# Performance work log

Hardware: AMD Instinct MI355X
Metric: run time of the kernel (lower is better)

Reference implementation:

```python
import jax, jax.numpy as jnp
import numpy as np
from jax import lax

B, C, H, W = 4, 512, 48, 48
R = 8            # inter_rate -> spatial q/k channels = C // R
C4 = C // 4      # chl_attention query channels
N = H * W


def _conv1x1(x, w, b=None):
    # x: (B,C,H,W), w: (O,C)
    y = jnp.einsum('bchw,oc->bohw', x, w)
    if b is not None:
        y = y + b[None, :, None, None]
    return y


def _conv3x3(x, w):
    # w: (O,I,3,3), SAME padding, no bias
    return lax.conv_general_dilated(x, w, (1, 1), 'SAME',
                                    dimension_numbers=('NCHW', 'OIHW', 'NCHW'))


def _bn_relu(x, scale, bias):
    # eval-mode BatchNorm folded into per-channel scale/bias, then ReLU
    return jax.nn.relu(x * scale[None, :, None, None] + bias[None, :, None, None])


def _masked_softmax(e, mask):
    # softmax restricted to mask>0 positions (== exp(e)*mask / sum(exp(e)*mask))
    neg = jnp.finfo(e.dtype).min
    z = jnp.where(mask[None] > 0, e, neg)
    return jax.nn.softmax(z, axis=-1)


def _chl(x, qw, qs, qb, ew, eb):
    # channel attention block (chl_attention)
    b, c, h, w = x.shape
    n = h * w
    q = jnp.einsum('bchw,oc->bohw', x, qw)                 # (B,C4,H,W)
    q = jax.nn.relu(q * qs[None, :, None, None] + qb[None, :, None, None])
    q = q.reshape(b, C4, n)
    k = x.reshape(b, c, n)
    energy = jnp.einsum('bqn,bcn->bqc', q, k)              # (B,C4,C)
    expand = jnp.einsum('oq,bqc->boc', ew, energy) + eb[None, :, None]  # (B,C,C)
    en = jnp.max(expand, -1, keepdims=True) - expand
    attn = jax.nn.softmax(en, -1)                          # (B,C,C)
    out = jnp.einsum('bcd,bdn->bcn', attn, k)
    return out.reshape(b, c, h, w)


def setup_inputs() -> dict:
    key = jax.random.key(0)
    ks = jax.random.split(key, 32)
    f = jnp.float32
    s = lambda k, shp, sc: (sc * jax.random.normal(k, shp)).astype(f)
    inp = {}
    inp['x'] = s(ks[0], (B, C, H, W), 1.0)
    Cr = C // R
    inp['wq'] = s(ks[1], (Cr, C), 1.0 / np.sqrt(C))
    inp['bq'] = s(ks[2], (Cr,), 0.02)
    inp['wk'] = s(ks[3], (Cr, C), 1.0 / np.sqrt(C))
    inp['bk'] = s(ks[4], (Cr,), 0.02)
    inp['wv0'] = s(ks[5], (C, C), 1.0 / np.sqrt(C))
    inp['bv0'] = s(ks[6], (C,), 0.02)
    inp['conv1_w'] = s(ks[7], (C, C, 3, 3), 1.0 / np.sqrt(9 * C))
    inp['conv1_s'] = (1.0 + 0.1 * jax.random.normal(ks[8], (C,))).astype(f)
    inp['conv1_b'] = s(ks[9], (C,), 0.05)
    inp['conv2_w'] = s(ks[10], (C, C, 3, 3), 1.0 / np.sqrt(9 * C))
    inp['conv2_s'] = (1.0 + 0.1 * jax.random.normal(ks[11], (C,))).astype(f)
    inp['conv2_b'] = s(ks[12], (C,), 0.05)
    inp['gamma'] = jnp.full((1,), 0.5, f)
    inp['gamma1'] = jnp.full((1,), 0.5, f)
    inp['gamma2'] = jnp.full((1,), 0.5, f)
    # chl_attention #1 params
    inp['c1_qw'] = s(ks[13], (C4, C), 1.0 / np.sqrt(C))
    inp['c1_qs'] = (1.0 + 0.1 * jax.random.normal(ks[14], (C4,))).astype(f)
    inp['c1_qb'] = s(ks[15], (C4,), 0.05)
    inp['c1_ew'] = s(ks[16], (C, C4), 1.0 / np.sqrt(C4))
    inp['c1_eb'] = s(ks[17], (C,), 0.02)
    # chl_attention #2 params
    inp['c2_qw'] = s(ks[18], (C4, C), 1.0 / np.sqrt(C))
    inp['c2_qs'] = (1.0 + 0.1 * jax.random.normal(ks[19], (C4,))).astype(f)
    inp['c2_qb'] = s(ks[20], (C4,), 0.05)
    inp['c2_ew'] = s(ks[21], (C, C4), 1.0 / np.sqrt(C4))
    inp['c2_eb'] = s(ks[22], (C,), 0.02)
    # binary (N,N) masks: random sparsity + diagonal so every row has support
    eye = jnp.eye(N, dtype=f)
    m1 = (jax.random.uniform(ks[23], (N, N)) < 0.25).astype(f)
    m2 = (jax.random.uniform(ks[24], (N, N)) < 0.10).astype(f)
    inp['mask1'] = jnp.maximum(m1, eye)
    inp['mask2'] = jnp.maximum(m2, eye)
    return inp


def reference(x, wq, bq, wk, bk, wv0, bv0, conv1_w, conv1_s, conv1_b,
              conv2_w, conv2_s, conv2_b, gamma, gamma1, gamma2,
              c1_qw, c1_qs, c1_qb, c1_ew, c1_eb,
              c2_qw, c2_qs, c2_qb, c2_ew, c2_eb, mask1, mask2):
    b, c, h, w = x.shape
    n = h * w
    q = _conv1x1(x, wq, bq).reshape(b, -1, n)   # (B,Cr,N)
    k = _conv1x1(x, wk, bk).reshape(b, -1, n)   # (B,Cr,N)
    energy = jnp.einsum('bqn,bqm->bnm', q, k)   # (B,N,N)
    attn0 = jax.nn.softmax(energy, -1)
    attn1 = _masked_softmax(energy, mask1)
    attn2 = _masked_softmax(energy, mask2)
    v = _conv1x1(x, wv0, bv0).reshape(b, c, n)
    # pass 0 (unmasked)
    out0 = jnp.einsum('bcn,bmn->bcm', v, attn0).reshape(b, c, h, w)
    out0 = gamma[0] * out0 + x
    out0 = _bn_relu(_conv3x3(out0, conv1_w), conv1_s, conv1_b)
    # pass 1 (mask1, channel-attn value)
    v1 = _chl(out0, c1_qw, c1_qs, c1_qb, c1_ew, c1_eb).reshape(b, c, n)
    out1 = jnp.einsum('bcn,bmn->bcm', v1, attn1).reshape(b, c, h, w)
    out1 = gamma1[0] * out1 + out0
    out1 = _bn_relu(_conv3x3(out1, conv2_w), conv2_s, conv2_b)
    # pass 2 (mask2)
    v2 = _chl(out1, c2_qw, c2_qs, c2_qb, c2_ew, c2_eb).reshape(b, c, n)
    out2 = jnp.einsum('bcn,bmn->bcm', v2, attn2).reshape(b, c, h, w)
    out = gamma2[0] * out2 + out1
    return out
```

## Files before the change

### kernel.cpp

```cpp
#include <hip/hip_runtime.h>

#define B_  4
#define C_  512
#define H_  48
#define W_  48
#define N_  2304
#define CR_ 64
#define C4_ 128
#define TK  16
#define LDSP 68
#define PW  50
#define PN  2500
#define KW  4608

typedef short  s16x8 __attribute__((ext_vector_type(8)));
typedef float  f32x4 __attribute__((ext_vector_type(4)));

__device__ __forceinline__ unsigned short f2bf(float f) {
  union { float f; unsigned int u; } v; v.f = f;
  const unsigned int u = v.u;
  return (unsigned short)((u + 0x7FFFu + ((u >> 16) & 1u)) >> 16);
}
__device__ __forceinline__ float bf2f(unsigned short h) {
  union { unsigned int u; float f; } v; v.u = ((unsigned int)h) << 16;
  return v.f;
}

__device__ __forceinline__ float blockReduceMax(float v, float* red) {
  const int tid = threadIdx.x;
  red[tid] = v; __syncthreads();
  for (int s = 128; s > 0; s >>= 1) {
    if (tid < s) red[tid] = fmaxf(red[tid], red[tid + s]);
    __syncthreads();
  }
  float r = red[0]; __syncthreads();
  return r;
// ... 447 lines not shown
  unsigned short* Tlb = Tl + (size_t)b * N_ * C_;
  for (int cs = 0; cs < 8; ++cs) {
    const int c0 = cs * 64;
    __syncthreads();
#pragma unroll
    for (int i = 0; i < 16; ++i) {
      const int cc = i * 4 + (tid >> 6);
      t[cc][tid & 63] = Xb[(size_t)(c0 + cc) * N_ + n0 + (tid & 63)];
    }
    __syncthreads();
    const int cc = tid & 63;
#pragma unroll
    for (int i = 0; i < 16; ++i) {
      const int nn = i * 4 + (tid >> 6);
      const float v = t[cc][nn];
      const unsigned short hh = f2bf(v);
      Thb[(size_t)(n0 + nn) * C_ + c0 + cc] = hh;
      Tlb[(size_t)(n0 + nn) * C_ + c0 + cc] = f2bf(v - bf2f(hh));
    }
  }
}

__global__ __launch_bounds__(256)
void mfma_conv3(const unsigned short* __restrict__ Xh, const unsigned short* __restrict__ Xl,
                const unsigned short* __restrict__ Wh, const unsigned short* __restrict__ Wl,
                const float* __restrict__ sc, const float* __restrict__ bi,
                float* __restrict__ Y)
{
  __shared__ unsigned short Ah[128][72], Al[128][72];
  __shared__ unsigned short Bh[64][72], Bl[64][72];
  const int b  = blockIdx.z;
  const int m0 = blockIdx.y * 128, n0 = blockIdx.x * 64;
  const int tid  = threadIdx.x;
  const int lane = tid & 63, wave = tid >> 6;
  const int wm = wave >> 1, wn = wave & 1;
  const int lrow = lane & 15, lk8 = (lane >> 4) * 8;
  const int aRow = tid >> 1, aK = (tid & 1) * 32;
  const int bRow = tid >> 2, bK = (tid & 3) * 16;
  const int nj = n0 + bRow;
  const int pbase = (nj / 48 + 1) * PW + (nj % 48) + 1;
  const unsigned short* Xhb = Xh + (size_t)b * PN * C_;
  const unsigned short* Xlb = Xl + (size_t)b * PN * C_;
  f32x4 acc[4][2] = {};
  s16x8 a0h, a1h, a2h, a3h, a0l, a1l, a2l, a3l, b0h, b1h, b0l, b1l;

#define CONV_LD(IT)                                                             \
  {                                                                             \
    const int tap_ = (IT) >> 3, c0_ = ((IT) & 7) * 64;                          \
    const int t3_ = tap_ / 3;                                                   \
    const int toff_ = (t3_ - 1) * PW + (tap_ - t3_ * 3 - 1);                    \
    const size_t bofs_ = (size_t)(pbase + toff_) * C_ + c0_ + bK;               \
    const size_t wrow_ = (size_t)(m0 + aRow) * KW + (size_t)tap_ * C_ + c0_ + aK; \
    a0h = *(const s16x8*)(Wh + wrow_);      a1h = *(const s16x8*)(Wh + wrow_ + 8);  \
    a2h = *(const s16x8*)(Wh + wrow_ + 16); a3h = *(const s16x8*)(Wh + wrow_ + 24); \
    a0l = *(const s16x8*)(Wl + wrow_);      a1l = *(const s16x8*)(Wl + wrow_ + 8);  \
    a2l = *(const s16x8*)(Wl + wrow_ + 16); a3l = *(const s16x8*)(Wl + wrow_ + 24); \
    b0h = *(const s16x8*)(Xhb + bofs_);     b1h = *(const s16x8*)(Xhb + bofs_ + 8); \
    b0l = *(const s16x8*)(Xlb + bofs_);     b1l = *(const s16x8*)(Xlb + bofs_ + 8); \
  }

  CONV_LD(0);
  for (int it = 0; it < 72; ++it) {
    *(s16x8*)&Ah[aRow][aK]      = a0h; *(s16x8*)&Ah[aRow][aK + 8]  = a1h;
    *(s16x8*)&Ah[aRow][aK + 16] = a2h; *(s16x8*)&Ah[aRow][aK + 24] = a3h;
    *(s16x8*)&Al[aRow][aK]      = a0l; *(s16x8*)&Al[aRow][aK + 8]  = a1l;
    *(s16x8*)&Al[aRow][aK + 16] = a2l; *(s16x8*)&Al[aRow][aK + 24] = a3l;
    *(s16x8*)&Bh[bRow][bK]      = b0h; *(s16x8*)&Bh[bRow][bK + 8]  = b1h;
    *(s16x8*)&Bl[bRow][bK]      = b0l; *(s16x8*)&Bl[bRow][bK + 8]  = b1l;
    __syncthreads();
    if (it < 71) CONV_LD(it + 1);
#pragma unroll
    for (int kc = 0; kc < 2; ++kc) {
      s16x8 ah[4], al[4], bh[2], bl[2];
#pragma unroll
      for (int mt = 0; mt < 4; ++mt) {
        ah[mt] = *(const s16x8*)&Ah[wm * 64 + mt * 16 + lrow][kc * 32 + lk8];
        al[mt] = *(const s16x8*)&Al[wm * 64 + mt * 16 + lrow][kc * 32 + lk8];
      }
#pragma unroll
      for (int nt = 0; nt < 2; ++nt) {
        bh[nt] = *(const s16x8*)&Bh[wn * 32 + nt * 16 + lrow][kc * 32 + lk8];
        bl[nt] = *(const s16x8*)&Bl[wn * 32 + nt * 16 + lrow][kc * 32 + lk8];
      }
#pragma unroll
      for (int mt = 0; mt < 4; ++mt)
#pragma unroll
        for (int nt = 0; nt < 2; ++nt) {
          acc[mt][nt] = __builtin_amdgcn_mfma_f32_16x16x32_bf16(ah[mt], bh[nt], acc[mt][nt], 0, 0, 0);
          acc[mt][nt] = __builtin_amdgcn_mfma_f32_16x16x32_bf16(ah[mt], bl[nt], acc[mt][nt], 0, 0, 0);
          acc[mt][nt] = __builtin_amdgcn_mfma_f32_16x16x32_bf16(al[mt], bh[nt], acc[mt][nt], 0, 0, 0);
        }
    }
    __syncthreads();
  }
#undef CONV_LD

  float* Yb = Y + (size_t)b * C_ * N_;
#pragma unroll
  for (int mt = 0; mt < 4; ++mt)
#pragma unroll
    for (int nt = 0; nt < 2; ++nt) {
      const int col = n0 + wn * 32 + nt * 16 + lrow;
      const int rbase = m0 + wm * 64 + mt * 16 + (lane >> 4) * 4;
#pragma unroll
      for (int i = 0; i < 4; ++i) {
        const int row = rbase + i;
        const float v = fmaxf(acc[mt][nt][i] * sc[row] + bi[row], 0.f);
        Yb[(size_t)row * N_ + col] = v;
      }
    }
}

__global__ __launch_bounds__(256)
void mfma_apply(const unsigned short* __restrict__ V, const float* __restrict__ E,
                const float* __restrict__ st, int variant,
                const float* __restrict__ mask,
                const float* __restrict__ gammaPtr,
                const float* __restrict__ Resid, float* __restrict__ Y)
{
  __shared__ unsigned short As[128][72];
  __shared__ unsigned short Bs[64][72];
  const int b  = blockIdx.z;
  const int c0 = blockIdx.y * 128, m0 = blockIdx.x * 64;
  const int tid  = threadIdx.x;
  const int lane = tid & 63, wave = tid >> 6;
  const int wm = wave >> 1, wn = wave & 1;
  const int lrow = lane & 15, lk8 = (lane >> 4) * 8;
  const int aRow = tid >> 1, aK = (tid & 1) * 32;
  const int bRow = tid >> 2, bK = (tid & 3) * 16;
  const int mrow = m0 + bRow;
  const float* sp = st + ((size_t)b * N_ + mrow) * 6 + variant * 2;
  const float mx = sp[0], rs = 1.f / sp[1];
  const unsigned short* Vb = V + (size_t)b * C_ * N_;
  const float* Er = E + ((size_t)b * N_ + mrow) * N_;
  const float* Mr = mask ? mask + (size_t)mrow * N_ : nullptr;
  f32x4 acc[4][2] = {};
  s16x8 a0, a1, a2, a3;
  float4 e0, e1, e2, e3, q0, q1, q2, q3;

#define APPLY_LD(K0)                                                      \
  {                                                                       \
    const unsigned short* s = Vb + (size_t)(c0 + aRow) * N_ + (K0) + aK;  \
    a0 = *(const s16x8*)(s);      a1 = *(const s16x8*)(s + 8);            \
    a2 = *(const s16x8*)(s + 16); a3 = *(const s16x8*)(s + 24);           \
    const float* e = Er + (K0) + bK;                                      \
    e0 = *(const float4*)(e);     e1 = *(const float4*)(e + 4);           \
    e2 = *(const float4*)(e + 8); e3 = *(const float4*)(e + 12);          \
    if (Mr) {                                                             \
      const float* m = Mr + (K0) + bK;                                    \
      q0 = *(const float4*)(m);     q1 = *(const float4*)(m + 4);         \
      q2 = *(const float4*)(m + 8); q3 = *(const float4*)(m + 12);        \
    }                                                                     \
  }

  APPLY_LD(0);
  for (int k0 = 0; k0 < N_; k0 += 64) {
    *(s16x8*)&As[aRow][aK]      = a0; *(s16x8*)&As[aRow][aK + 8]  = a1;
    *(s16x8*)&As[aRow][aK + 16] = a2; *(s16x8*)&As[aRow][aK + 24] = a3;
    {
      float w[16];
      const float4 ee[4] = {e0, e1, e2, e3};
      const float4 qq[4] = {q0, q1, q2, q3};
#pragma unroll
      for (int g4 = 0; g4 < 4; ++g4) {
        const float4 e4 = ee[g4];
        w[g4 * 4 + 0] = __expf(e4.x - mx) * rs;
        w[g4 * 4 + 1] = __expf(e4.y - mx) * rs;
        w[g4 * 4 + 2] = __expf(e4.z - mx) * rs;
        w[g4 * 4 + 3] = __expf(e4.w - mx) * rs;
        if (Mr) {
          const float4 m4 = qq[g4];
          if (!(m4.x > 0.f)) w[g4 * 4 + 0] = 0.f;
          if (!(m4.y > 0.f)) w[g4 * 4 + 1] = 0.f;
          if (!(m4.z > 0.f)) w[g4 * 4 + 2] = 0.f;
          if (!(m4.w > 0.f)) w[g4 * 4 + 3] = 0.f;
        }
      }
      s16x8 p0, p1;
#pragma unroll
      for (int t = 0; t < 8; ++t) { p0[t] = (short)f2bf(w[t]); p1[t] = (short)f2bf(w[8 + t]); }
      *(s16x8*)&Bs[bRow][bK]     = p0;
      *(s16x8*)&Bs[bRow][bK + 8] = p1;
    }
    __syncthreads();
    if (k0 + 64 < N_) APPLY_LD(k0 + 64);
#pragma unroll
    for (int kc = 0; kc < 2; ++kc) {
      s16x8 av[4], bv[2];
#pragma unroll
      for (int mt = 0; mt < 4; ++mt)
        av[mt] = *(const s16x8*)&As[wm * 64 + mt * 16 + lrow][kc * 32 + lk8];
#pragma unroll
      for (int nt = 0; nt < 2; ++nt)
        bv[nt] = *(const s16x8*)&Bs[wn * 32 + nt * 16 + lrow][kc * 32 + lk8];
#pragma unroll
      for (int mt = 0; mt < 4; ++mt)
#pragma unroll
        for (int nt = 0; nt < 2; ++nt)
          acc[mt][nt] = __builtin_amdgcn_mfma_f32_16x16x32_bf16(av[mt], bv[nt], acc[mt][nt], 0, 0, 0);
    }
    __syncthreads();
  }
#undef APPLY_LD

  const float g = gammaPtr[0];
  float* Yb = Y + (size_t)b * C_ * N_;
  const float* Rb = Resid + (size_t)b * C_ * N_;
#pragma unroll
  for (int mt = 0; mt < 4; ++mt)
#pragma unroll
    for (int nt = 0; nt < 2; ++nt) {
      const int col = m0 + wn * 32 + nt * 16 + lrow;
      const int rbase = c0 + wm * 64 + mt * 16 + (lane >> 4) * 4;
#pragma unroll
      for (int i = 0; i < 4; ++i) {
        const int row = rbase + i;
        const size_t off = (size_t)row * N_ + col;
        Yb[off] = g * acc[mt][nt][i] + Rb[off];
      }
    }
}

__global__ __launch_bounds__(256)
void mfma_conv_split(const float* __restrict__ X, const float* __restrict__ Wt,
                     const float* __restrict__ sc, const float* __restrict__ bi,
                     float* __restrict__ Y)
{
  __shared__ unsigned short Ah[64][72], Al[64][72];
  __shared__ unsigned short Bh[64][72], Bl[64][72];
  const int b  = blockIdx.z;
  const int m0 = blockIdx.y * 64, n0 = blockIdx.x * 64;
  const int tid  = threadIdx.x;
  const int lane = tid & 63, wave = tid >> 6;
  const int wm = wave >> 1, wn = wave & 1;
  const int lrow = lane & 15, lk8 = (lane >> 4) * 8;
  const int sRow = tid >> 2, sK = (tid & 3) * 16;
  const int tj = tid & 63, tkg = (tid >> 6) * 16;
  const int n = n0 + tj, yy = n / W_, xx = n - yy * W_;
  const float* Xb = X + (size_t)b * C_ * N_;
  f32x4 acc[2][2] = {};

  for (int k0 = 0; k0 < KW; k0 += 64) {
    {
      const float* src = Wt + (size_t)(m0 + sRow) * KW + k0 + sK;
      unsigned short h[16], l[16];
#pragma unroll
      for (int t = 0; t < 16; ++t) {
        const float v = src[t];
        const unsigned short hh = f2bf(v);
        h[t] = hh;
        l[t] = f2bf(v - bf2f(hh));
      }
      *(s16x8*)&Ah[sRow][sK]     = *(s16x8*)&h[0];
      *(s16x8*)&Ah[sRow][sK + 8] = *(s16x8*)&h[8];
      *(s16x8*)&Al[sRow][sK]     = *(s16x8*)&l[0];
      *(s16x8*)&Al[sRow][sK + 8] = *(s16x8*)&l[8];
    }
    {
#pragma unroll
      for (int ii = 0; ii < 16; ii += 2) {
        unsigned int ph = 0, pl = 0;
#pragma unroll
        for (int hft = 0; hft < 2; ++hft) {
          const int kg = k0 + tkg + ii + hft;
          const int c = kg / 9, tap = kg - c * 9;
          const int t3 = tap / 3;
          const int iy = yy + t3 - 1, ix = xx + (tap - t3 * 3) - 1;
          float v = 0.f;
          if (iy >= 0 && iy < H_ && ix >= 0 && ix < W_)
            v = Xb[(size_t)c * N_ + iy * W_ + ix];
          const unsigned short hh = f2bf(v);
          const unsigned short ll = f2bf(v - bf2f(hh));
          ph |= ((unsigned int)hh) << (16 * hft);
          pl |= ((unsigned int)ll) << (16 * hft);
        }
        *(unsigned int*)&Bh[tj][tkg + ii] = ph;
        *(unsigned int*)&Bl[tj][tkg + ii] = pl;
      }
    }
    __syncthreads();
#pragma unroll
    for (int kc = 0; kc < 2; ++kc) {
      const s16x8 ah0 = *(const s16x8*)&Ah[wm * 32 + lrow     ][kc * 32 + lk8];
      const s16x8 ah1 = *(const s16x8*)&Ah[wm * 32 + 16 + lrow][kc * 32 + lk8];
      const s16x8 al0 = *(const s16x8*)&Al[wm * 32 + lrow     ][kc * 32 + lk8];
      const s16x8 al1 = *(const s16x8*)&Al[wm * 32 + 16 + lrow][kc * 32 + lk8];
      const s16x8 bh0 = *(const s16x8*)&Bh[wn * 32 + lrow     ][kc * 32 + lk8];
      const s16x8 bh1 = *(const s16x8*)&Bh[wn * 32 + 16 + lrow][kc * 32 + lk8];
      const s16x8 bl0 = *(const s16x8*)&Bl[wn * 32 + lrow     ][kc * 32 + lk8];
      const s16x8 bl1 = *(const s16x8*)&Bl[wn * 32 + 16 + lrow][kc * 32 + lk8];
      acc[0][0] = __builtin_amdgcn_mfma_f32_16x16x32_bf16(ah0, bh0, acc[0][0], 0, 0, 0);
      acc[0][1] = __builtin_amdgcn_mfma_f32_16x16x32_bf16(ah0, bh1, acc[0][1], 0, 0, 0);
      acc[1][0] = __builtin_amdgcn_mfma_f32_16x16x32_bf16(ah1, bh0, acc[1][0], 0, 0, 0);
      acc[1][1] = __builtin_amdgcn_mfma_f32_16x16x32_bf16(ah1, bh1, acc[1][1], 0, 0, 0);
      acc[0][0] = __builtin_amdgcn_mfma_f32_16x16x32_bf16(ah0, bl0, acc[0][0], 0, 0, 0);
      acc[0][1] = __builtin_amdgcn_mfma_f32_16x16x32_bf16(ah0, bl1, acc[0][1], 0, 0, 0);
      acc[1][0] = __builtin_amdgcn_mfma_f32_16x16x32_bf16(ah1, bl0, acc[1][0], 0, 0, 0);
      acc[1][1] = __builtin_amdgcn_mfma_f32_16x16x32_bf16(ah1, bl1, acc[1][1], 0, 0, 0);
      acc[0][0] = __builtin_amdgcn_mfma_f32_16x16x32_bf16(al0, bh0, acc[0][0], 0, 0, 0);
      acc[0][1] = __builtin_amdgcn_mfma_f32_16x16x32_bf16(al0, bh1, acc[0][1], 0, 0, 0);
      acc[1][0] = __builtin_amdgcn_mfma_f32_16x16x32_bf16(al1, bh0, acc[1][0], 0, 0, 0);
      acc[1][1] = __builtin_amdgcn_mfma_f32_16x16x32_bf16(al1, bh1, acc[1][1], 0, 0, 0);
    }
    __syncthreads();
  }

  float* Yb = Y + (size_t)b * C_ * N_;
#pragma unroll
  for (int mt = 0; mt < 2; ++mt)
#pragma unroll
    for (int nt = 0; nt < 2; ++nt) {
      const int col = n0 + wn * 32 + nt * 16 + lrow;
      const int rbase = m0 + wm * 32 + mt * 16 + (lane >> 4) * 4;
#pragma unroll
      for (int i = 0; i < 4; ++i) {
        const int row = rbase + i;
        const float v = fmaxf(acc[mt][nt][i] * sc[row] + bi[row], 0.f);
        Yb[(size_t)row * N_ + col] = v;
      }
    }
}

__global__ __launch_bounds__(256)
void softmax_stats(const float* __restrict__ E, const float* __restrict__ M1,
                   const float* __restrict__ M2, float* __restrict__ st)
{
  const int row = blockIdx.x, b = blockIdx.y, tid = threadIdx.x;
  const float* er = E + ((size_t)b * N_ + row) * N_;
  const float* r1 = M1 + (size_t)row * N_;
  const float* r2 = M2 + (size_t)row * N_;
  float mx0 = -3.4e38f, mx1 = -3.4e38f, mx2 = -3.4e38f;
  for (int n = tid; n < N_; n += 256) {
    const float v = er[n];
    mx0 = fmaxf(mx0, v);
    if (r1[n] > 0.f) mx1 = fmaxf(mx1, v);
    if (r2[n] > 0.f) mx2 = fmaxf(mx2, v);
  }
  __shared__ float red[256];
  mx0 = blockReduceMax(mx0, red);
  mx1 = blockReduceMax(mx1, red);
  mx2 = blockReduceMax(mx2, red);
  float s0 = 0.f, s1 = 0.f, s2 = 0.f;
  for (int n = tid; n < N_; n += 256) {
// ... 250 lines not shown
  const float* c2ew   = (const float*)d_in[24];
  const float* c2eb   = (const float*)d_in[25];
  const float* mask1  = (const float*)d_in[26];
  const float* mask2  = (const float*)d_in[27];

  const size_t QK = 589824;
  const size_t CQ = 1179648;
  const size_t VV = 4718592;
  const size_t EE = 21233664;
  const size_t ST = 55296;
  const size_t CE = 262144;
  const size_t CA = 1048576;
  const size_t ELEMS_B = CQ + VV + EE + ST + VV + CE + CA;
  const size_t ELEMS_A = ELEMS_B + EE / 2;
  const int tier = (ws_size >= ELEMS_A * 4) ? 0
                 : (ws_size >= ELEMS_B * 4) ? 1 : 2;

  float* ws = (float*)d_ws;
  float *qbuf, *kbuf, *cq, *vbuf, *ebuf, *stb, *o0, *ce1, *cat_;
  unsigned short *Xh = nullptr, *Xl = nullptr,
                 *W1h = nullptr, *W1l = nullptr, *W2h = nullptr, *W2l = nullptr,
                 *xTh = nullptr, *xTl = nullptr, *oTh = nullptr, *oTl = nullptr;
  float *qTf = nullptr, *kTf = nullptr;
  if (tier <= 1) {
    qbuf = ws; kbuf = ws + QK;
    cq   = ws;
    vbuf = ws + CQ;
    ebuf = vbuf + VV;
    stb  = ebuf + EE;
    o0   = stb + ST;
    ce1  = o0 + VV;
    cat_ = ce1 + CE;
    if (tier == 0) {
      unsigned short* reg = (unsigned short*)(cat_ + CA);
      xTh = reg;
      xTl = reg + 4718592;
      qTf = (float*)(reg + 9437184);
      kTf = qTf + 589824;
      W1h = reg + 11796480;
      W1l = reg + 14155776;
      W2h = reg + 16515072;
      W2l = reg + 18874368;
      Xh  = reg;
      Xl  = reg + 5120000;
      oTh = reg;
      oTl = reg + 4718592;
    }
  } else {
    qbuf = ws; kbuf = qbuf + QK;
    cq   = kbuf + QK;
    vbuf = cq + CQ;
    stb  = vbuf + VV;
    o0   = stb + ST;
    ce1  = o0 + VV;
    cat_ = ce1 + CE;
    ebuf = nullptr;
  }
  float* t0 = (float*)d_out;
  unsigned short* vb16 = (unsigned short*)vbuf;

  const dim3 TPB(256);
  const long long sxc = (long long)C_ * N_;
  const long long sqr = (long long)CR_ * N_;
  const long long sq4 = (long long)C4_ * N_;
  const long long sNN = (long long)N_ * N_;
  const long long sNC = (long long)N_ * C_;
  const long long sCC = (long long)C_ * C_;
  const long long sEC = (long long)C4_ * C_;
  const long long sNR = (long long)N_ * CR_;

  if (tier == 0) {
    tr_split<<<dim3(B_, 36), TPB, 0, stream>>>(x, xTh, xTl);
    mfma_sp<<<dim3(36, 1, 4), TPB, 0, stream>>>(wq, 0, C_, xTh, xTl, sNC, C_, 1,
        qTf, sNR, CR_, 1, C_, 1, nullptr, bq, 0);
    mfma_sp<<<dim3(36, 1, 4), TPB, 0, stream>>>(wk, 0, C_, xTh, xTl, sNC, C_, 1,
        kTf, sNR, CR_, 1, C_, 1, nullptr, bk, 0);
    mfma_gemm<<<dim3(36, 8, 4), TPB, 0, stream>>>(wv0, 0, 0, C_, xTh, sNC, C_, 2,
        vb16, 1, sxc, N_, C_, nullptr, bv0, 0, nullptr, nullptr, 0);
    mfma_sp<<<dim3(36, 36, 4), TPB, 0, stream>>>(qTf, sNR, CR_, kTf, nullptr, sNR, CR_, 0,
        ebuf, sNN, N_, 0, CR_, 1, nullptr, nullptr, 0);
    softmax_stats<<<dim3(N_, 4), TPB, 0, stream>>>(ebuf, mask1, mask2, stb);
    wsplit<<<dim3(512, 9), TPB, 0, stream>>>(c1w, W1h, W1l);
    wsplit<<<dim3(512, 9), TPB, 0, stream>>>(c2w, W2h, W2l);
  } else if (tier == 1) {
    gemm_nn<<<dim3(36, 1, 4), TPB, 0, stream>>>(wq, 0, C_, x, sxc, N_,
                                                qbuf, sqr, N_, C_, nullptr, bq, 0);
    gemm_nn<<<dim3(36, 1, 4), TPB, 0, stream>>>(wk, 0, C_, x, sxc, N_,
                                                kbuf, sqr, N_, C_, nullptr, bk, 0);
    mfma_gemm<<<dim3(36, 8, 4), TPB, 0, stream>>>(wv0, 0, 0, C_, x, sxc, N_, 1,
        vbuf, 0, sxc, N_, C_, nullptr, bv0, 0, nullptr, nullptr, 0);
    gemm_tn<<<dim3(36, 36, 4), TPB, 0, stream>>>(qbuf, sqr, N_, kbuf, sqr, N_,
                                                 ebuf, sNN, N_, CR_);
    softmax_stats<<<dim3(N_, 4), TPB, 0, stream>>>(ebuf, mask1, mask2, stb);
  } else {
    gemm_nn<<<dim3(36, 1, 4), TPB, 0, stream>>>(wq, 0, C_, x, sxc, N_,
                                                qbuf, sqr, N_, C_, nullptr, bq, 0);
    gemm_nn<<<dim3(36, 1, 4), TPB, 0, stream>>>(wk, 0, C_, x, sxc, N_,
                                                kbuf, sqr, N_, C_, nullptr, bk, 0);
    mfma_gemm<<<dim3(36, 8, 4), TPB, 0, stream>>>(wv0, 0, 0, C_, x, sxc, N_, 1,
        vbuf, 0, sxc, N_, C_, nullptr, bv0, 0, nullptr, nullptr, 0);
    softmax_stats_rq<<<dim3(N_, 4), TPB, 0, stream>>>(qbuf, kbuf, mask1, mask2, stb);
  }

  for (int pass = 0; pass < 3; ++pass) {
    const float* msk = (pass == 0) ? nullptr : (pass == 1 ? mask1 : mask2);
    const float* gm  = (pass == 0) ? gamma : (pass == 1 ? gamma1 : gamma2);
    const float* res = (pass == 0) ? x : o0;
    float* dst = (pass == 2) ? (float*)d_out : t0;

    if (tier == 0) {
      mfma_apply<<<dim3(36, 4, 4), TPB, 0, stream>>>(vb16, ebuf, stb, pass, msk,
                                                     gm, res, dst);
    } else if (tier == 1) {
      attn_apply<<<dim3(36, 8, 4), TPB, 0, stream>>>(vbuf, ebuf, stb, pass, msk,
                                                     gm, res, dst);
    } else {
      attn_apply_rq<<<dim3(36, 8, 4), TPB, 0, stream>>>(vbuf, qbuf, kbuf, stb, pass, msk,
                                                        gm, res, dst);
    }
    if (pass == 2) break;

    const float* cs = (pass == 0) ? c1s : c2s;
    const float* cb = (pass == 0) ? c1b : c2b;
    if (tier == 0) {
      pad_split2<<<dim3(B_, 37), TPB, 0, stream>>>(dst, Xh, Xl);
      mfma_conv3<<<dim3(36, 4, 4), TPB, 0, stream>>>(Xh, Xl,
          (pass == 0) ? W1h : W2h, (pass == 0) ? W1l : W2l, cs, cb, o0);
    } else {
      const float* cw = (pass == 0) ? c1w : c2w;
      mfma_conv_split<<<dim3(36, 8, 4), TPB, 0, stream>>>(dst, cw, cs, cb, o0);
    }

    const float* qw = (pass == 0) ? c1qw : c2qw;
    const float* qs = (pass == 0) ? c1qs : c2qs;
    const float* qb = (pass == 0) ? c1qb : c2qb;
    const float* ew = (pass == 0) ? c1ew : c2ew;
    const float* eb = (pass == 0) ? c1eb : c2eb;
    if (tier == 0) {
      tr_split<<<dim3(B_, 36), TPB, 0, stream>>>(o0, oTh, oTl);
      mfma_sp<<<dim3(36, 2, 4), TPB, 0, stream>>>(qw, 0, C_, oTh, oTl, sNC, C_, 1,
          cq, sq4, N_, 0, C_, 1, qs, qb, 1);
      zero_buf<<<dim3(256), TPB, 0, stream>>>((float4*)ce1, (int)(CE / 4));
      mfma_sp<<<dim3(8, 2, 16), TPB, 0, stream>>>(cq, sq4, N_, o0, nullptr, sxc, N_, 0,
          ce1, sEC, C4_, 2, N_, 4, nullptr, nullptr, 0);
      mfma_sp<<<dim3(8, 8, 4), TPB, 0, stream>>>(ew, 0, C4_, ce1, nullptr, sEC, C4_, 0,
          cat_, sCC, C_, 0, C4_, 1, nullptr, eb, 0);
      chl_softmax<<<dim3(C_ * 4), TPB, 0, stream>>>(cat_);
      mfma_gemm<<<dim3(36, 8, 4), TPB, 0, stream>>>(cat_, 0, sCC, C_, oTh, sNC, C_, 2,
          vb16, 1, sxc, N_, C_, nullptr, nullptr, 0, nullptr, nullptr, 0);
// ... 15 lines not shown
```

Measured before the change: 1.283 ms.

## Pack attention masks into bitmasks and switch conv to 64-row tiles

Adds a mask_pack kernel that turns each float mask row into 64-bit ballot words. The softmax stats kernel and the attention apply kernel now read these bits instead of float masks, which cuts mask memory traffic by about 32x in the masked passes. The 3x3 conv goes back to a 64x64 output tile (mfma_conv2, grid 36x8x4) in place of the 128x64 tile, giving more blocks and fewer registers per block but less reuse of each loaded tile. Two extra small pack launches are added.

Result: faster. 1.222 ms (-4.8%).

```diff
diff --git a/kernel.cpp b/kernel.cpp
--- a/kernel.cpp
+++ b/kernel.cpp
@@ -12,6 +12,7 @@
 #define PW  50
 #define PN  2500
 #define KW  4608
+#define NW  36
 
 typedef short  s16x8 __attribute__((ext_vector_type(8)));
 typedef float  f32x4 __attribute__((ext_vector_type(4)));
@@ -505,209 +506,23 @@
 }
 
 __global__ __launch_bounds__(256)
-void mfma_conv3(const unsigned short* __restrict__ Xh, const unsigned short* __restrict__ Xl,
+void mask_pack(const float* __restrict__ M, unsigned long long* __restrict__ Mb)
+{
+  const int row = blockIdx.x;
+  const int tid = threadIdx.x, lane = tid & 63, wv = tid >> 6;
+  const float* r = M + (size_t)row * N_;
+  unsigned long long* o = Mb + (size_t)row * NW;
+  for (int i = wv; i < NW; i += 4) {
+    const unsigned long long m = __ballot(r[i * 64 + lane] > 0.f);
+    if (lane == 0) o[i] = m;
+  }
+}
+
+__global__ __launch_bounds__(256)
+void mfma_conv2(const unsigned short* __restrict__ Xh, const unsigned short* __restrict__ Xl,
                 const unsigned short* __restrict__ Wh, const unsigned short* __restrict__ Wl,
                 const float* __restrict__ sc, const float* __restrict__ bi,
                 float* __restrict__ Y)
-{
-  __shared__ unsigned short Ah[128][72], Al[128][72];
-  __shared__ unsigned short Bh[64][72], Bl[64][72];
-  const int b  = blockIdx.z;
-  const int m0 = blockIdx.y * 128, n0 = blockIdx.x * 64;
-  const int tid  = threadIdx.x;
-  const int lane = tid & 63, wave = tid >> 6;
-  const int wm = wave >> 1, wn = wave & 1;
-  const int lrow = lane & 15, lk8 = (lane >> 4) * 8;
-  const int aRow = tid >> 1, aK = (tid & 1) * 32;
-  const int bRow = tid >> 2, bK = (tid & 3) * 16;
-  const int nj = n0 + bRow;
-  const int pbase = (nj / 48 + 1) * PW + (nj % 48) + 1;
-  const unsigned short* Xhb = Xh + (size_t)b * PN * C_;
-  const unsigned short* Xlb = Xl + (size_t)b * PN * C_;
-  f32x4 acc[4][2] = {};
-  s16x8 a0h, a1h, a2h, a3h, a0l, a1l, a2l, a3l, b0h, b1h, b0l, b1l;
-
-#define CONV_LD(IT)                                                             \
-  {                                                                             \
-    const int tap_ = (IT) >> 3, c0_ = ((IT) & 7) * 64;                          \
-    const int t3_ = tap_ / 3;                                                   \
-    const int toff_ = (t3_ - 1) * PW + (tap_ - t3_ * 3 - 1);                    \
-    const size_t bofs_ = (size_t)(pbase + toff_) * C_ + c0_ + bK;               \
-    const size_t wrow_ = (size_t)(m0 + aRow) * KW + (size_t)tap_ * C_ + c0_ + aK; \
-    a0h = *(const s16x8*)(Wh + wrow_);      a1h = *(const s16x8*)(Wh + wrow_ + 8);  \
-    a2h = *(const s16x8*)(Wh + wrow_ + 16); a3h = *(const s16x8*)(Wh + wrow_ + 24); \
-    a0l = *(const s16x8*)(Wl + wrow_);      a1l = *(const s16x8*)(Wl + wrow_ + 8);  \
-    a2l = *(const s16x8*)(Wl + wrow_ + 16); a3l = *(const s16x8*)(Wl + wrow_ + 24); \
-    b0h = *(const s16x8*)(Xhb + bofs_);     b1h = *(const s16x8*)(Xhb + bofs_ + 8); \
-    b0l = *(const s16x8*)(Xlb + bofs_);     b1l = *(const s16x8*)(Xlb + bofs_ + 8); \
-  }
-
-  CONV_LD(0);
-  for (int it = 0; it < 72; ++it) {
-    *(s16x8*)&Ah[aRow][aK]      = a0h; *(s16x8*)&Ah[aRow][aK + 8]  = a1h;
-    *(s16x8*)&Ah[aRow][aK + 16] = a2h; *(s16x8*)&Ah[aRow][aK + 24] = a3h;
-    *(s16x8*)&Al[aRow][aK]      = a0l; *(s16x8*)&Al[aRow][aK + 8]  = a1l;
-    *(s16x8*)&Al[aRow][aK + 16] = a2l; *(s16x8*)&Al[aRow][aK + 24] = a3l;
-    *(s16x8*)&Bh[bRow][bK]      = b0h; *(s16x8*)&Bh[bRow][bK + 8]  = b1h;
-    *(s16x8*)&Bl[bRow][bK]      = b0l; *(s16x8*)&Bl[bRow][bK + 8]  = b1l;
-    __syncthreads();
-    if (it < 71) CONV_LD(it + 1);
-#pragma unroll
-    for (int kc = 0; kc < 2; ++kc) {
-      s16x8 ah[4], al[4], bh[2], bl[2];
-#pragma unroll
-      for (int mt = 0; mt < 4; ++mt) {
-        ah[mt] = *(const s16x8*)&Ah[wm * 64 + mt * 16 + lrow][kc * 32 + lk8];
-        al[mt] = *(const s16x8*)&Al[wm * 64 + mt * 16 + lrow][kc * 32 + lk8];
-      }
-#pragma unroll
-      for (int nt = 0; nt < 2; ++nt) {
-        bh[nt] = *(const s16x8*)&Bh[wn * 32 + nt * 16 + lrow][kc * 32 + lk8];
-        bl[nt] = *(const s16x8*)&Bl[wn * 32 + nt * 16 + lrow][kc * 32 + lk8];
-      }
-#pragma unroll
-      for (int mt = 0; mt < 4; ++mt)
-#pragma unroll
-        for (int nt = 0; nt < 2; ++nt) {
-          acc[mt][nt] = __builtin_amdgcn_mfma_f32_16x16x32_bf16(ah[mt], bh[nt], acc[mt][nt], 0, 0, 0);
-          acc[mt][nt] = __builtin_amdgcn_mfma_f32_16x16x32_bf16(ah[mt], bl[nt], acc[mt][nt], 0, 0, 0);
-          acc[mt][nt] = __builtin_amdgcn_mfma_f32_16x16x32_bf16(al[mt], bh[nt], acc[mt][nt], 0, 0, 0);
-        }
-    }
-    __syncthreads();
-  }
-#undef CONV_LD
-
-  float* Yb = Y + (size_t)b * C_ * N_;
-#pragma unroll
-  for (int mt = 0; mt < 4; ++mt)
-#pragma unroll
-    for (int nt = 0; nt < 2; ++nt) {
-      const int col = n0 + wn * 32 + nt * 16 + lrow;
-      const int rbase = m0 + wm * 64 + mt * 16 + (lane >> 4) * 4;
-#pragma unroll
-      for (int i = 0; i < 4; ++i) {
-        const int row = rbase + i;
-        const float v = fmaxf(acc[mt][nt][i] * sc[row] + bi[row], 0.f);
-        Yb[(size_t)row * N_ + col] = v;
-      }
-    }
-}
-
-__global__ __launch_bounds__(256)
-void mfma_apply(const unsigned short* __restrict__ V, const float* __restrict__ E,
-                const float* __restrict__ st, int variant,
-                const float* __restrict__ mask,
-                const float* __restrict__ gammaPtr,
-                const float* __restrict__ Resid, float* __restrict__ Y)
-{
-  __shared__ unsigned short As[128][72];
-  __shared__ unsigned short Bs[64][72];
-  const int b  = blockIdx.z;
-  const int c0 = blockIdx.y * 128, m0 = blockIdx.x * 64;
-  const int tid  = threadIdx.x;
-  const int lane = tid & 63, wave = tid >> 6;
-  const int wm = wave >> 1, wn = wave & 1;
-  const int lrow = lane & 15, lk8 = (lane >> 4) * 8;
-  const int aRow = tid >> 1, aK = (tid & 1) * 32;
-  const int bRow = tid >> 2, bK = (tid & 3) * 16;
-  const int mrow = m0 + bRow;
-  const float* sp = st + ((size_t)b * N_ + mrow) * 6 + variant * 2;
-  const float mx = sp[0], rs = 1.f / sp[1];
-  const unsigned short* Vb = V + (size_t)b * C_ * N_;
-  const float* Er = E + ((size_t)b * N_ + mrow) * N_;
-  const float* Mr = mask ? mask + (size_t)mrow * N_ : nullptr;
-  f32x4 acc[4][2] = {};
-  s16x8 a0, a1, a2, a3;
-  float4 e0, e1, e2, e3, q0, q1, q2, q3;
-
-#define APPLY_LD(K0)                                                      \
-  {                                                                       \
-    const unsigned short* s = Vb + (size_t)(c0 + aRow) * N_ + (K0) + aK;  \
-    a0 = *(const s16x8*)(s);      a1 = *(const s16x8*)(s + 8);            \
-    a2 = *(const s16x8*)(s + 16); a3 = *(const s16x8*)(s + 24);           \
-    const float* e = Er + (K0) + bK;                                      \
-    e0 = *(const float4*)(e);     e1 = *(const float4*)(e + 4);           \
-    e2 = *(const float4*)(e + 8); e3 = *(const float4*)(e + 12);          \
-    if (Mr) {                                                             \
-      const float* m = Mr + (K0) + bK;                                    \
-      q0 = *(const float4*)(m);     q1 = *(const float4*)(m + 4);         \
-      q2 = *(const float4*)(m + 8); q3 = *(const float4*)(m + 12);        \
-    }                                                                     \
-  }
-
-  APPLY_LD(0);
-  for (int k0 = 0; k0 < N_; k0 += 64) {
-    *(s16x8*)&As[aRow][aK]      = a0; *(s16x8*)&As[aRow][aK + 8]  = a1;
-    *(s16x8*)&As[aRow][aK + 16] = a2; *(s16x8*)&As[aRow][aK + 24] = a3;
-    {
-      float w[16];
-      const float4 ee[4] = {e0, e1, e2, e3};
-      const float4 qq[4] = {q0, q1, q2, q3};
-#pragma unroll
-      for (int g4 = 0; g4 < 4; ++g4) {
-        const float4 e4 = ee[g4];
-        w[g4 * 4 + 0] = __expf(e4.x - mx) * rs;
-        w[g4 * 4 + 1] = __expf(e4.y - mx) * rs;
-        w[g4 * 4 + 2] = __expf(e4.z - mx) * rs;
-        w[g4 * 4 + 3] = __expf(e4.w - mx) * rs;
-        if (Mr) {
-          const float4 m4 = qq[g4];
-          if (!(m4.x > 0.f)) w[g4 * 4 + 0] = 0.f;
-          if (!(m4.y > 0.f)) w[g4 * 4 + 1] = 0.f;
-          if (!(m4.z > 0.f)) w[g4 * 4 + 2] = 0.f;
-          if (!(m4.w > 0.f)) w[g4 * 4 + 3] = 0.f;
-        }
-      }
-      s16x8 p0, p1;
-#pragma unroll
-      for (int t = 0; t < 8; ++t) { p0[t] = (short)f2bf(w[t]); p1[t] = (short)f2bf(w[8 + t]); }
-      *(s16x8*)&Bs[bRow][bK]     = p0;
-      *(s16x8*)&Bs[bRow][bK + 8] = p1;
-    }
-    __syncthreads();
-    if (k0 + 64 < N_) APPLY_LD(k0 + 64);
-#pragma unroll
-    for (int kc = 0; kc < 2; ++kc) {
-      s16x8 av[4], bv[2];
-#pragma unroll
-      for (int mt = 0; mt < 4; ++mt)
-        av[mt] = *(const s16x8*)&As[wm * 64 + mt * 16 + lrow][kc * 32 + lk8];
-#pragma unroll
-      for (int nt = 0; nt < 2; ++nt)
-        bv[nt] = *(const s16x8*)&Bs[wn * 32 + nt * 16 + lrow][kc * 32 + lk8];
-#pragma unroll
-      for (int mt = 0; mt < 4; ++mt)
-#pragma unroll
-        for (int nt = 0; nt < 2; ++nt)
-          acc[mt][nt] = __builtin_amdgcn_mfma_f32_16x16x32_bf16(av[mt], bv[nt], acc[mt][nt], 0, 0, 0);
-    }
-    __syncthreads();
-  }
-#undef APPLY_LD
-
-  const float g = gammaPtr[0];
-  float* Yb = Y + (size_t)b * C_ * N_;
-  const float* Rb = Resid + (size_t)b * C_ * N_;
-#pragma unroll
-  for (int mt = 0; mt < 4; ++mt)
-#pragma unroll
-    for (int nt = 0; nt < 2; ++nt) {
-      const int col = m0 + wn * 32 + nt * 16 + lrow;
-      const int rbase = c0 + wm * 64 + mt * 16 + (lane >> 4) * 4;
-#pragma unroll
-      for (int i = 0; i < 4; ++i) {
-        const int row = rbase + i;
-        const size_t off = (size_t)row * N_ + col;
-        Yb[off] = g * acc[mt][nt][i] + Rb[off];
-      }
-    }
-}
-
-__global__ __launch_bounds__(256)
-void mfma_conv_split(const float* __restrict__ X, const float* __restrict__ Wt,
-                     const float* __restrict__ sc, const float* __restrict__ bi,
-                     float* __restrict__ Y)
 {
   __shared__ unsigned short Ah[64][72], Al[64][72];
   __shared__ unsigned short Bh[64][72], Bl[64][72];
@@ -718,50 +533,34 @@
   const int wm = wave >> 1, wn = wave & 1;
   const int lrow = lane & 15, lk8 = (lane >> 4) * 8;
   const int sRow = tid >> 2, sK = (tid & 3) * 16;
-  const int tj = tid & 63, tkg = (tid >> 6) * 16;
-  const int n = n0 + tj, yy = n / W_, xx = n - yy * W_;
-  const float* Xb = X + (size_t)b * C_ * N_;
+  const int nj = n0 + sRow;
+  const int pbase = (nj / 48 + 1) * PW + (nj % 48) + 1;
+  const unsigned short* Xhb = Xh + (size_t)b * PN * C_;
+  const unsigned short* Xlb = Xl + (size_t)b * PN * C_;
   f32x4 acc[2][2] = {};
-
-  for (int k0 = 0; k0 < KW; k0 += 64) {
-    {
-      const float* src = Wt + (size_t)(m0 + sRow) * KW + k0 + sK;
-      unsigned short h[16], l[16];
-#pragma unroll
-      for (int t = 0; t < 16; ++t) {
-        const float v = src[t];
-        const unsigned short hh = f2bf(v);
-        h[t] = hh;
-        l[t] = f2bf(v - bf2f(hh));
-      }
-      *(s16x8*)&Ah[sRow][sK]     = *(s16x8*)&h[0];
-      *(s16x8*)&Ah[sRow][sK + 8] = *(s16x8*)&h[8];
-      *(s16x8*)&Al[sRow][sK]     = *(s16x8*)&l[0];
-      *(s16x8*)&Al[sRow][sK + 8] = *(s16x8*)&l[8];
-    }
-    {
-#pragma unroll
-      for (int ii = 0; ii < 16; ii += 2) {
-        unsigned int ph = 0, pl = 0;
-#pragma unroll
-        for (int hft = 0; hft < 2; ++hft) {
-          const int kg = k0 + tkg + ii + hft;
-          const int c = kg / 9, tap = kg - c * 9;
-          const int t3 = tap / 3;
-          const int iy = yy + t3 - 1, ix = xx + (tap - t3 * 3) - 1;
-          float v = 0.f;
-          if (iy >= 0 && iy < H_ && ix >= 0 && ix < W_)
-            v = Xb[(size_t)c * N_ + iy * W_ + ix];
-          const unsigned short hh = f2bf(v);
-          const unsigned short ll = f2bf(v - bf2f(hh));
-          ph |= ((unsigned int)hh) << (16 * hft);
-          pl |= ((unsigned int)ll) << (16 * hft);
-        }
-        *(unsigned int*)&Bh[tj][tkg + ii] = ph;
-        *(unsigned int*)&Bl[tj][tkg + ii] = pl;
-      }
-    }
-    __syncthreads();
+  s16x8 r0, r1, r2, r3, r4, r5, r6, r7;
+
+#define CONV_LD(IT)                                                        \
+  {                                                                        \
+    const int tap_ = (IT) >> 3, c0_ = ((IT) & 7) * 64;                     \
+    const int t3_ = tap_ / 3;                                              \
+    const int toff_ = (t3_ - 1) * PW + (tap_ - t3_ * 3 - 1);               \
+    const size_t bofs_ = (size_t)(pbase + toff_) * C_ + c0_ + sK;          \
+    const size_t wrow_ = (size_t)(m0 + sRow) * KW + (size_t)tap_ * C_ + c0_ + sK; \
+    r0 = *(const s16x8*)(Wh + wrow_);     r1 = *(const s16x8*)(Wh + wrow_ + 8); \
+    r2 = *(const s16x8*)(Wl + wrow_);     r3 = *(const s16x8*)(Wl + wrow_ + 8); \
+    r4 = *(const s16x8*)(Xhb + bofs_);    r5 = *(const s16x8*)(Xhb + bofs_ + 8); \
+    r6 = *(const s16x8*)(Xlb + bofs_);    r7 = *(const s16x8*)(Xlb + bofs_ + 8); \
+  }
+
+  CONV_LD(0);
+  for (int it = 0; it < 72; ++it) {
+    *(s16x8*)&Ah[sRow][sK] = r0; *(s16x8*)&Ah[sRow][sK + 8] = r1;
+    *(s16x8*)&Al[sRow][sK] = r2; *(s16x8*)&Al[sRow][sK + 8] = r3;
+    *(s16x8*)&Bh[sRow][sK] = r4; *(s16x8*)&Bh[sRow][sK + 8] = r5;
+    *(s16x8*)&Bl[sRow][sK] = r6; *(s16x8*)&Bl[sRow][sK + 8] = r7;
+    __syncthreads();
+    if (it < 71) CONV_LD(it + 1);
 #pragma unroll
     for (int kc = 0; kc < 2; ++kc) {
       const s16x8 ah0 = *(const s16x8*)&Ah[wm * 32 + lrow     ][kc * 32 + lk8];
@@ -787,6 +586,7 @@
     }
     __syncthreads();
   }
+#undef CONV_LD
 
   float* Yb = Y + (size_t)b * C_ * N_;
 #pragma unroll
@@ -802,6 +602,255 @@
         Yb[(size_t)row * N_ + col] = v;
       }
     }
+}
+
+__global__ __launch_bounds__(256)
+void mfma_apply(const unsigned short* __restrict__ V, const float* __restrict__ E,
+                const float* __restrict__ st, int variant,
+                const unsigned long long* __restrict__ Mb,
+                const float* __restrict__ gammaPtr,
+                const float* __restrict__ Resid, float* __restrict__ Y)
+{
+  __shared__ unsigned short As[128][72];
+  __shared__ unsigned short Bs[64][72];
+  const int b  = blockIdx.z;
+  const int c0 = blockIdx.y * 128, m0 = blockIdx.x * 64;
+  const int tid  = threadIdx.x;
+  const int lane = tid & 63, wave = tid >> 6;
+  const int wm = wave >> 1, wn = wave & 1;
+  const int lrow = lane & 15, lk8 = (lane >> 4) * 8;
+  const int aRow = tid >> 1, aK = (tid & 1) * 32;
+  const int bRow = tid >> 2, bK = (tid & 3) * 16;
+  const int mrow = m0 + bRow;
+  const float* sp = st + ((size_t)b * N_ + mrow) * 6 + variant * 2;
+  const float mx = sp[0], rs = 1.f / sp[1];
+  const unsigned short* Vb = V + (size_t)b * C_ * N_;
+  const float* Er = E + ((size_t)b * N_ + mrow) * N_;
+  const unsigned long long* Mw = Mb ? Mb + (size_t)mrow * NW : nullptr;
+  f32x4 acc[4][2] = {};
+  s16x8 a0, a1, a2, a3;
+  float4 e0, e1, e2, e3;
+  unsigned long long mw = ~0ULL;
+
+#define APPLY_LD(K0)                                                      \
+  {                                                                       \
+    const unsigned short* s = Vb + (size_t)(c0 + aRow) * N_ + (K0) + aK;  \
+    a0 = *(const s16x8*)(s);      a1 = *(const s16x8*)(s + 8);            \
+    a2 = *(const s16x8*)(s + 16); a3 = *(const s16x8*)(s + 24);           \
+    const float* e = Er + (K0) + bK;                                      \
+    e0 = *(const float4*)(e);     e1 = *(const float4*)(e + 4);           \
+    e2 = *(const float4*)(e + 8); e3 = *(const float4*)(e + 12);          \
+    if (Mw) mw = Mw[(K0) >> 6];                                           \
+  }
+
+  APPLY_LD(0);
+  for (int k0 = 0; k0 < N_; k0 += 64) {
+    *(s16x8*)&As[aRow][aK]      = a0; *(s16x8*)&As[aRow][aK + 8]  = a1;
+    *(s16x8*)&As[aRow][aK + 16] = a2; *(s16x8*)&As[aRow][aK + 24] = a3;
+    {
+      float w[16];
+      const float4 ee[4] = {e0, e1, e2, e3};
+#pragma unroll
+      for (int g4 = 0; g4 < 4; ++g4) {
+        const float4 e4 = ee[g4];
+        w[g4 * 4 + 0] = __expf(e4.x - mx) * rs;
+        w[g4 * 4 + 1] = __expf(e4.y - mx) * rs;
+        w[g4 * 4 + 2] = __expf(e4.z - mx) * rs;
+        w[g4 * 4 + 3] = __expf(e4.w - mx) * rs;
+      }
+      if (Mw) {
+        const unsigned long long mm = mw;
+#pragma unroll
+        for (int t = 0; t < 16; ++t)
+          if (!((mm >> (bK + t)) & 1ULL)) w[t] = 0.f;
+      }
+      s16x8 p0, p1;
+#pragma unroll
+      for (int t = 0; t < 8; ++t) { p0[t] = (short)f2bf(w[t]); p1[t] = (short)f2bf(w[8 + t]); }
+      *(s16x8*)&Bs[bRow][bK]     = p0;
+      *(s16x8*)&Bs[bRow][bK + 8] = p1;
+    }
+    __syncthreads();
+    if (k0 + 64 < N_) APPLY_LD(k0 + 64);
+#pragma unroll
+    for (int kc = 0; kc < 2; ++kc) {
+      s16x8 av[4], bv[2];
+#pragma unroll
+      for (int mt = 0; mt < 4; ++mt)
+        av[mt] = *(const s16x8*)&As[wm * 64 + mt * 16 + lrow][kc * 32 + lk8];
+#pragma unroll
+      for (int nt = 0; nt < 2; ++nt)
+        bv[nt] = *(const s16x8*)&Bs[wn * 32 + nt * 16 + lrow][kc * 32 + lk8];
+#pragma unroll
+      for (int mt = 0; mt < 4; ++mt)
+#pragma unroll
+        for (int nt = 0; nt < 2; ++nt)
+          acc[mt][nt] = __builtin_amdgcn_mfma_f32_16x16x32_bf16(av[mt], bv[nt], acc[mt][nt], 0, 0, 0);
+    }
+    __syncthreads();
+  }
+#undef APPLY_LD
+
+  const float g = gammaPtr[0];
+  float* Yb = Y + (size_t)b * C_ * N_;
+  const float* Rb = Resid + (size_t)b * C_ * N_;
+#pragma unroll
+  for (int mt = 0; mt < 4; ++mt)
+#pragma unroll
+    for (int nt = 0; nt < 2; ++nt) {
+      const int col = m0 + wn * 32 + nt * 16 + lrow;
+      const int rbase = c0 + wm * 64 + mt * 16 + (lane >> 4) * 4;
+#pragma unroll
+      for (int i = 0; i < 4; ++i) {
+        const int row = rbase + i;
+        const size_t off = (size_t)row * N_ + col;
+        Yb[off] = g * acc[mt][nt][i] + Rb[off];
+      }
+    }
+}
+
+__global__ __launch_bounds__(256)
+void mfma_conv_split(const float* __restrict__ X, const float* __restrict__ Wt,
+                     const float* __restrict__ sc, const float* __restrict__ bi,
+                     float* __restrict__ Y)
+{
+  __shared__ unsigned short Ah[64][72], Al[64][72];
+  __shared__ unsigned short Bh[64][72], Bl[64][72];
+  const int b  = blockIdx.z;
+  const int m0 = blockIdx.y * 64, n0 = blockIdx.x * 64;
+  const int tid  = threadIdx.x;
+  const int lane = tid & 63, wave = tid >> 6;
+  const int wm = wave >> 1, wn = wave & 1;
+  const int lrow = lane & 15, lk8 = (lane >> 4) * 8;
+  const int sRow = tid >> 2, sK = (tid & 3) * 16;
+  const int tj = tid & 63, tkg = (tid >> 6) * 16;
+  const int n = n0 + tj, yy = n / W_, xx = n - yy * W_;
+  const float* Xb = X + (size_t)b * C_ * N_;
+  f32x4 acc[2][2] = {};
+
+  for (int k0 = 0; k0 < KW; k0 += 64) {
+    {
+      const float* src = Wt + (size_t)(m0 + sRow) * KW + k0 + sK;
+      unsigned short h[16], l[16];
+#pragma unroll
+      for (int t = 0; t < 16; ++t) {
+        const float v = src[t];
+        const unsigned short hh = f2bf(v);
+        h[t] = hh;
+        l[t] = f2bf(v - bf2f(hh));
+      }
+      *(s16x8*)&Ah[sRow][sK]     = *(s16x8*)&h[0];
+      *(s16x8*)&Ah[sRow][sK + 8] = *(s16x8*)&h[8];
+      *(s16x8*)&Al[sRow][sK]     = *(s16x8*)&l[0];
+      *(s16x8*)&Al[sRow][sK + 8] = *(s16x8*)&l[8];
+    }
+    {
+#pragma unroll
+      for (int ii = 0; ii < 16; ii += 2) {
+        unsigned int ph = 0, pl = 0;
+#pragma unroll
+        for (int hft = 0; hft < 2; ++hft) {
+          const int kg = k0 + tkg + ii + hft;
+          const int c = kg / 9, tap = kg - c * 9;
+          const int t3 = tap / 3;
+          const int iy = yy + t3 - 1, ix = xx + (tap - t3 * 3) - 1;
+          float v = 0.f;
+          if (iy >= 0 && iy < H_ && ix >= 0 && ix < W_)
+            v = Xb[(size_t)c * N_ + iy * W_ + ix];
+          const unsigned short hh = f2bf(v);
+          const unsigned short ll = f2bf(v - bf2f(hh));
+          ph |= ((unsigned int)hh) << (16 * hft);
+          pl |= ((unsigned int)ll) << (16 * hft);
+        }
+        *(unsigned int*)&Bh[tj][tkg + ii] = ph;
+        *(unsigned int*)&Bl[tj][tkg + ii] = pl;
+      }
+    }
+    __syncthreads();
+#pragma unroll
+    for (int kc = 0; kc < 2; ++kc) {
+      const s16x8 ah0 = *(const s16x8*)&Ah[wm * 32 + lrow     ][kc * 32 + lk8];
+      const s16x8 ah1 = *(const s16x8*)&Ah[wm * 32 + 16 + lrow][kc * 32 + lk8];
+      const s16x8 al0 = *(const s16x8*)&Al[wm * 32 + lrow     ][kc * 32 + lk8];
+      const s16x8 al1 = *(const s16x8*)&Al[wm * 32 + 16 + lrow][kc * 32 + lk8];
+      const s16x8 bh0 = *(const s16x8*)&Bh[wn * 32 + lrow     ][kc * 32 + lk8];
+      const s16x8 bh1 = *(const s16x8*)&Bh[wn * 32 + 16 + lrow][kc * 32 + lk8];
+      const s16x8 bl0 = *(const s16x8*)&Bl[wn * 32 + lrow     ][kc * 32 + lk8];
+      const s16x8 bl1 = *(const s16x8*)&Bl[wn * 32 + 16 + lrow][kc * 32 + lk8];
+      acc[0][0] = __builtin_amdgcn_mfma_f32_16x16x32_bf16(ah0, bh0, acc[0][0], 0, 0, 0);
+      acc[0][1] = __builtin_amdgcn_mfma_f32_16x16x32_bf16(ah0, bh1, acc[0][1], 0, 0, 0);
+      acc[1][0] = __builtin_amdgcn_mfma_f32_16x16x32_bf16(ah1, bh0, acc[1][0], 0, 0, 0);
+      acc[1][1] = __builtin_amdgcn_mfma_f32_16x16x32_bf16(ah1, bh1, acc[1][1], 0, 0, 0);
+      acc[0][0] = __builtin_amdgcn_mfma_f32_16x16x32_bf16(ah0, bl0, acc[0][0], 0, 0, 0);
+      acc[0][1] = __builtin_amdgcn_mfma_f32_16x16x32_bf16(ah0, bl1, acc[0][1], 0, 0, 0);
+      acc[1][0] = __builtin_amdgcn_mfma_f32_16x16x32_bf16(ah1, bl0, acc[1][0], 0, 0, 0);
+      acc[1][1] = __builtin_amdgcn_mfma_f32_16x16x32_bf16(ah1, bl1, acc[1][1], 0, 0, 0);
+      acc[0][0] = __builtin_amdgcn_mfma_f32_16x16x32_bf16(al0, bh0, acc[0][0], 0, 0, 0);
+      acc[0][1] = __builtin_amdgcn_mfma_f32_16x16x32_bf16(al0, bh1, acc[0][1], 0, 0, 0);
+      acc[1][0] = __builtin_amdgcn_mfma_f32_16x16x32_bf16(al1, bh0, acc[1][0], 0, 0, 0);
+      acc[1][1] = __builtin_amdgcn_mfma_f32_16x16x32_bf16(al1, bh1, acc[1][1], 0, 0, 0);
+    }
+    __syncthreads();
+  }
+
+  float* Yb = Y + (size_t)b * C_ * N_;
+#pragma unroll
+  for (int mt = 0; mt < 2; ++mt)
+#pragma unroll
+    for (int nt = 0; nt < 2; ++nt) {
+      const int col = n0 + wn * 32 + nt * 16 + lrow;
+      const int rbase = m0 + wm * 32 + mt * 16 + (lane >> 4) * 4;
+#pragma unroll
+      for (int i = 0; i < 4; ++i) {
+        const int row = rbase + i;
+        const float v = fmaxf(acc[mt][nt][i] * sc[row] + bi[row], 0.f);
+        Yb[(size_t)row * N_ + col] = v;
+      }
+    }
+}
+
+__global__ __launch_bounds__(256)
+void softmax_stats_bm(const float* __restrict__ E,
+                      const unsigned long long* __restrict__ M1b,
+                      const unsigned long long* __restrict__ M2b,
+                      float* __restrict__ st)
+{
+  const int row = blockIdx.x, b = blockIdx.y, tid = threadIdx.x;
+  const float* er = E + ((size_t)b * N_ + row) * N_;
+  const unsigned long long* r1 = M1b + (size_t)row * NW;
+  const unsigned long long* r2 = M2b + (size_t)row * NW;
+  const int bitp = tid & 63;
+  float ev[9];
+  bool f1[9], f2[9];
+  float mx0 = -3.4e38f, mx1 = -3.4e38f, mx2 = -3.4e38f;
+#pragma unroll
+  for (int i = 0; i < 9; ++i) {
+    const int n = tid + i * 256;
+    ev[i] = er[n];
+    f1[i] = (r1[n >> 6] >> bitp) & 1ULL;
+    f2[i] = (r2[n >> 6] >> bitp) & 1ULL;
+    mx0 = fmaxf(mx0, ev[i]);
+    if (f1[i]) mx1 = fmaxf(mx1, ev[i]);
+    if (f2[i]) mx2 = fmaxf(mx2, ev[i]);
+  }
+  __shared__ float red[256];
+  mx0 = blockReduceMax(mx0, red);
+  mx1 = blockReduceMax(mx1, red);
+  mx2 = blockReduceMax(mx2, red);
+  float s0 = 0.f, s1 = 0.f, s2 = 0.f;
+#pragma unroll
+  for (int i = 0; i < 9; ++i) {
+    s0 += __expf(ev[i] - mx0);
+    if (f1[i]) s1 += __expf(ev[i] - mx1);
+    if (f2[i]) s2 += __expf(ev[i] - mx2);
+  }
+  s0 = blockReduceSum(s0, red);
+  s1 = blockReduceSum(s1, red);
+  s2 = blockReduceSum(s2, red);
+  if (tid == 0) {
+    float* o = st + ((size_t)b * N_ + row) * 6;
+    o[0] = mx0; o[1] = s0; o[2] = mx1; o[3] = s1; o[4] = mx2; o[5] = s2;
+  }
 }
 
 __global__ __launch_bounds__(256)
@@ -1098,6 +1147,7 @@
                  *W1h = nullptr, *W1l = nullptr, *W2h = nullptr, *W2l = nullptr,
                  *xTh = nullptr, *xTl = nullptr, *oTh = nullptr, *oTl = nullptr;
   float *qTf = nullptr, *kTf = nullptr;
+  unsigned long long *Mb1 = nullptr, *Mb2 = nullptr;
   if (tier <= 1) {
     qbuf = ws; kbuf = ws + QK;
     cq   = ws;
@@ -1121,6 +1171,8 @@
       Xl  = reg + 5120000;
       oTh = reg;
       oTl = reg + 4718592;
+      Mb1 = (unsigned long long*)(reg + 10240000);
+      Mb2 = Mb1 + (size_t)N_ * NW;
     }
   } else {
     qbuf = ws; kbuf = qbuf + QK;
@@ -1155,7 +1207,9 @@
         vb16, 1, sxc, N_, C_, nullptr, bv0, 0, nullptr, nullptr, 0);
     mfma_sp<<<dim3(36, 36, 4), TPB, 0, stream>>>(qTf, sNR, CR_, kTf, nullptr, sNR, CR_, 0,
         ebuf, sNN, N_, 0, CR_, 1, nullptr, nullptr, 0);
-    softmax_stats<<<dim3(N_, 4), TPB, 0, stream>>>(ebuf, mask1, mask2, stb);
+    mask_pack<<<dim3(N_), TPB, 0, stream>>>(mask1, Mb1);
+    mask_pack<<<dim3(N_), TPB, 0, stream>>>(mask2, Mb2);
+    softmax_stats_bm<<<dim3(N_, 4), TPB, 0, stream>>>(ebuf, Mb1, Mb2, stb);
     wsplit<<<dim3(512, 9), TPB, 0, stream>>>(c1w, W1h, W1l);
     wsplit<<<dim3(512, 9), TPB, 0, stream>>>(c2w, W2h, W2l);
   } else if (tier == 1) {
@@ -1180,12 +1234,13 @@
 
   for (int pass = 0; pass < 3; ++pass) {
     const float* msk = (pass == 0) ? nullptr : (pass == 1 ? mask1 : mask2);
+    const unsigned long long* mbk = (pass == 0) ? nullptr : (pass == 1 ? Mb1 : Mb2);
     const float* gm  = (pass == 0) ? gamma : (pass == 1 ? gamma1 : gamma2);
     const float* res = (pass == 0) ? x : o0;
     float* dst = (pass == 2) ? (float*)d_out : t0;
 
     if (tier == 0) {
-      mfma_apply<<<dim3(36, 4, 4), TPB, 0, stream>>>(vb16, ebuf, stb, pass, msk,
+      mfma_apply<<<dim3(36, 4, 4), TPB, 0, stream>>>(vb16, ebuf, stb, pass, mbk,
                                                      gm, res, dst);
     } else if (tier == 1) {
       attn_apply<<<dim3(36, 8, 4), TPB, 0, stream>>>(vbuf, ebuf, stb, pass, msk,
@@ -1200,7 +1255,7 @@
     const float* cb = (pass == 0) ? c1b : c2b;
     if (tier == 0) {
       pad_split2<<<dim3(B_, 37), TPB, 0, stream>>>(dst, Xh, Xl);
-      mfma_conv3<<<dim3(36, 4, 4), TPB, 0, stream>>>(Xh, Xl,
+      mfma_conv2<<<dim3(36, 8, 4), TPB, 0, stream>>>(Xh, Xl,
           (pass == 0) ? W1h : W2h, (pass == 0) ? W1l : W2l, cs, cb, o0);
     } else {
       const float* cw = (pass == 0) ? c1w : c2w;
```
